# Kernel optimization log

Hardware: AMD Instinct MI355X
Metric: run time of the kernel (lower is better)

Reference implementation:

```python
import jax, jax.numpy as jnp
import numpy as np

D, H = 64, 16
B, S = 4, 4096
PI = 3.1415  # constant used verbatim in the original code


def setup_inputs() -> dict:
    key = jax.random.key(0)
    ks = jax.random.split(key, 11)
    inp = {
        'query': jax.random.normal(ks[0], (B, S, D), dtype=jnp.float32),
        'key': jax.random.normal(ks[1], (B, S, D), dtype=jnp.float32),
        'value': jax.random.normal(ks[2], (B, S, D), dtype=jnp.float32),
        'attn_mask': jnp.zeros((1,), dtype=bool),
        # Linear weights stored as (in, out); y = x @ W + b
        'wq_w': jax.random.normal(ks[3], (D, D * H), dtype=jnp.float32) * 0.05,
        'wq_b': jnp.zeros((D * H,), dtype=jnp.float32),
        'wk_w': jax.random.normal(ks[4], (D, D * H), dtype=jnp.float32) * 0.05,
        'wk_b': jnp.zeros((D * H,), dtype=jnp.float32),
        'wv_w': jax.random.normal(ks[5], (D, D * H), dtype=jnp.float32) * 0.05,
        'wv_b': jnp.zeros((D * H,), dtype=jnp.float32),
        'dense_w': jax.random.normal(ks[6], (D * H, D), dtype=jnp.float32) * 0.05,
        'dense_b': jnp.zeros((D,), dtype=jnp.float32),
    }
    return inp


def reference(query, key, value, attn_mask, wq_w, wq_b, wk_w, wk_b, wv_w, wv_b, dense_w, dense_b):
    b, s, _ = query.shape
    # projections -> (B, S, H, D); einsum axis n = heads
    q = (query @ wq_w + wq_b).reshape(b, s, H, D)
    k = (key @ wk_w + wk_b).reshape(b, s, H, D)
    v = (value @ wv_w + wv_b).reshape(b, s, H, D)

    q = jax.nn.elu(q) + 1.0
    k = jax.nn.elu(k) + 1.0

    pos = PI * jnp.arange(s, dtype=query.dtype) / s  # (S,)
    qc_w = jnp.cos(pos)
    qs_w = jnp.sin(pos)
    kc_w = jnp.sin(pos)  # NB: original uses sin for k_cos too (faithful)
    ks_w = jnp.sin(pos)

    q_cos = q * qc_w[None, :, None, None]
    q_sin = q * qs_w[None, :, None, None]
    k_cos = k * kc_w[None, :, None, None]
    k_sin = k * ks_w[None, :, None, None]

    def lin_attn(qf, kf):
        kv = jnp.einsum('bsnx,bsnz->bnxz', kf, v)      # (B,H,D,D)
        return jnp.einsum('bsnx,bnxz->bsnz', qf, kv)   # (B,S,H,D)

    qkv = lin_attn(q, k)
    qkv_cos = lin_attn(q_cos, k_cos)
    qkv_sin = lin_attn(q_sin, k_sin)

    denom = 1.0 / (
        jnp.einsum('bsnd,bnd->bsn', q, k.sum(axis=1))
        + jnp.einsum('bsnd,bnd->bsn', q_cos, k_cos.sum(axis=1))
        + jnp.einsum('bsnd,bnd->bsn', q_sin, k_sin.sum(axis=1))
        + 1e-05
    )

    O = (qkv + qkv_cos + qkv_sin) * denom[..., None]   # (B,S,H,D)
    concat = O.reshape(b, s, H * D)
    return concat @ dense_w + dense_b
```

## Files before the change

### kernel.cpp

```cpp
#include <hip/hip_runtime.h>
#include <math.h>

#define BB 4
#define SS 4096
#define DD 64
#define HH 16
#define PI_C 3.1415f


typedef __attribute__((ext_vector_type(8))) short short8;
typedef __attribute__((ext_vector_type(4))) float f32x4;

#define MFMA(a, b, c) __builtin_amdgcn_mfma_f32_16x16x32_bf16(a, b, c, 0, 0, 0)

__device__ __forceinline__ short f2bf(float f) {
    union { float f; unsigned u; } v; v.f = f;
    unsigned r = v.u + 0x7FFFu + ((v.u >> 16) & 1u);
    return (short)(r >> 16);
}
__device__ __forceinline__ float bf2f(short s) {
    union { unsigned u; float f; } v;
    v.u = ((unsigned)(unsigned short)s) << 16;
    return v.f;
}
__device__ __forceinline__ short8 cvt8(float4 a, float4 b) {
    short8 r;
    r[0] = f2bf(a.x); r[1] = f2bf(a.y); r[2] = f2bf(a.z); r[3] = f2bf(a.w);
    r[4] = f2bf(b.x); r[5] = f2bf(b.y); r[6] = f2bf(b.z); r[7] = f2bf(b.w);
    return r;
}
__device__ __forceinline__ float elu1(float x) { return x > 0.f ? x + 1.f : __expf(x); }
__device__ __forceinline__ void st4(short* p, short a, short b, short c, short d) {
    union { uint2 u; short s[4]; } x;
    x.s[0] = a; x.s[1] = b; x.s[2] = c; x.s[3] = d;
    *reinterpret_cast<uint2*>(p) = x.u;
}

__global__ __launch_bounds__(256) void k_prep(
    const float* __restrict__ wq, const float* __restrict__ wk,
    const float* __restrict__ wv, const float* __restrict__ wd,
    short* __restrict__ dst)
{
    const int h = blockIdx.x, y = blockIdx.y, t = threadIdx.x;
    const float* src = (y == 0) ? wq : (y == 1) ? wk : (y == 2) ? wv : wd;
    const int rs = (y < 3) ? 1024 : 64;
    const size_t srcbase = (y < 3) ? (size_t)(h * 64) : (size_t)(h * 4096);
    short* dm = dst + (size_t)y * 65536 + (size_t)h * 4096;
#pragma unroll
    for (int j = 0; j < 4; ++j) {
        int idx = j * 1024 + t * 4;
        int r = idx >> 6, c = idx & 63;
        float4 v = *reinterpret_cast<const float4*>(src + (size_t)r * rs + srcbase + c);
        dm[(c + 0) * 64 + r] = f2bf(v.x);
        dm[(c + 1) * 64 + r] = f2bf(v.y);
        dm[(c + 2) * 64 + r] = f2bf(v.z);
        dm[(c + 3) * 64 + r] = f2bf(v.w);
    }
}

__global__ __launch_bounds__(256, 2) void k_phase1(
    const float* __restrict__ key, const float* __restrict__ value,
    const float* __restrict__ wk_b, const float* __restrict__ wv_b,
    const short* __restrict__ wkTb, const short* __restrict__ wvTb,
    float* __restrict__ pkv, float* __restrict__ pkvs,
    float* __restrict__ pks)
{
    const int chunk = blockIdx.x, h = blockIdx.y, b = blockIdx.z;
    const int t = threadIdx.x, w = t >> 6, l = t & 63;
    const int lane15 = l & 15, q8 = (l >> 4) * 8, q4 = (l >> 4) * 4;

    __shared__ short kT[2][64 * 72], vT[2][64 * 72], vsT[2][64 * 72];
    __shared__ float ssin[512];
    __shared__ float sbk[64], sbv[64];
    __shared__ float sred[512];

    short8 bkf[2][4], bvf[2][4];
    {
        const short* wkh = wkTb + (size_t)h * 4096;
        const short* wvh = wvTb + (size_t)h * 4096;
#pragma unroll
        for (int kss = 0; kss < 2; ++kss)
#pragma unroll
            for (int nt = 0; nt < 4; ++nt) {
                bkf[kss][nt] = *reinterpret_cast<const short8*>(wkh + (nt * 16 + lane15) * 64 + kss * 32 + q8);
                bvf[kss][nt] = *reinterpret_cast<const short8*>(wvh + (nt * 16 + lane15) * 64 + kss * 32 + q8);
            }
    }
    ssin[t]       = __sinf(PI_C * (float)(chunk * 512 + t)       * (1.f / 4096.f));
    ssin[t + 256] = __sinf(PI_C * (float)(chunk * 512 + t + 256) * (1.f / 4096.f));
    if (t < 64) sbk[t] = wk_b[h * 64 + t];
    else if (t < 128) sbv[t - 64] = wv_b[h * 64 + (t - 64)];

    float4 kf0, kf1, kf2, kf3, vf0, vf1, vf2, vf3;
    {
        const size_t g = ((size_t)b * SS + chunk * 512 + w * 16 + lane15) * 64 + q8;
        kf0 = *reinterpret_cast<const float4*>(key + g);
        kf1 = *reinterpret_cast<const float4*>(key + g + 4);
        kf2 = *reinterpret_cast<const float4*>(key + g + 32);
        kf3 = *reinterpret_cast<const float4*>(key + g + 36);
        vf0 = *reinterpret_cast<const float4*>(value + g);
        vf1 = *reinterpret_cast<const float4*>(value + g + 4);
        vf2 = *reinterpret_cast<const float4*>(value + g + 32);
        vf3 = *reinterpret_cast<const float4*>(value + g + 36);
    }

    f32x4 ckv[4], ckvs[4];
#pragma unroll
    for (int i = 0; i < 4; ++i) {
        ckv[i]  = (f32x4){0.f, 0.f, 0.f, 0.f};
        ckvs[i] = (f32x4){0.f, 0.f, 0.f, 0.f};
    }
    float aks = 0.f, akss = 0.f;

    auto proj_store = [&](int buf, int sbase) {
        f32x4 ckp[4], cvp[4];
#pragma unroll
        for (int i = 0; i < 4; ++i) {
            ckp[i] = (f32x4){0.f, 0.f, 0.f, 0.f};
            cvp[i] = (f32x4){0.f, 0.f, 0.f, 0.f};
        }
        short8 ak0 = cvt8(kf0, kf1), ak1 = cvt8(kf2, kf3);
        short8 av0 = cvt8(vf0, vf1), av1 = cvt8(vf2, vf3);
#pragma unroll
        for (int nt = 0; nt < 4; ++nt) {
            ckp[nt] = MFMA(ak0, bkf[0][nt], ckp[nt]);
            cvp[nt] = MFMA(av0, bvf[0][nt], cvp[nt]);
            ckp[nt] = MFMA(ak1, bkf[1][nt], ckp[nt]);
            cvp[nt] = MFMA(av1, bvf[1][nt], cvp[nt]);
        }
        const int srel = w * 16 + q4;
#pragma unroll
        for (int nt = 0; nt < 4; ++nt) {
            const int x = nt * 16 + lane15;
            const float bk = sbk[x], bv = sbv[x];
            short ek[4], ev[4], es[4];
#pragma unroll
            for (int r = 0; r < 4; ++r) {
                float kk = elu1(ckp[nt][r] + bk);
                float vv = cvp[nt][r] + bv;
                ek[r] = f2bf(kk);
                ev[r] = f2bf(vv);
                es[r] = f2bf(vv * ssin[sbase + srel + r]);
            }
            st4(&kT [buf][x * 72 + srel], ek[0], ek[1], ek[2], ek[3]);
            st4(&vT [buf][x * 72 + srel], ev[0], ev[1], ev[2], ev[3]);
            st4(&vsT[buf][x * 72 + srel], es[0], es[1], es[2], es[3]);
        }
    };

    __syncthreads();
    proj_store(0, 0);
    __syncthreads();

#pragma unroll 1
    for (int it = 0; it < 8; ++it) {
        const int cur = it & 1;
        if (it < 7) {
            const size_t g = ((size_t)b * SS + chunk * 512 + (it + 1) * 64 + w * 16 + lane15) * 64 + q8;
            kf0 = *reinterpret_cast<const float4*>(key + g);
            kf1 = *reinterpret_cast<const float4*>(key + g + 4);
            kf2 = *reinterpret_cast<const float4*>(key + g + 32);
            kf3 = *reinterpret_cast<const float4*>(key + g + 36);
            vf0 = *reinterpret_cast<const float4*>(value + g);
            vf1 = *reinterpret_cast<const float4*>(value + g + 4);
            vf2 = *reinterpret_cast<const float4*>(value + g + 32);
            vf3 = *reinterpret_cast<const float4*>(value + g + 36);
        }
#pragma unroll
        for (int kstep = 0; kstep < 2; ++kstep) {
            const int so = kstep * 32;
            short8 aV  = *reinterpret_cast<const short8*>(&vT [cur][(w * 16 + lane15) * 72 + so + q8]);
            short8 aVS = *reinterpret_cast<const short8*>(&vsT[cur][(w * 16 + lane15) * 72 + so + q8]);
#pragma unroll
            for (int nt = 0; nt < 4; ++nt) {
                short8 bK = *reinterpret_cast<const short8*>(&kT[cur][(nt * 16 + lane15) * 72 + so + q8]);
                ckv[nt]  = MFMA(aV,  bK, ckv[nt]);
                ckvs[nt] = MFMA(aVS, bK, ckvs[nt]);
            }
        }
        {
            const int sbase = it * 64;
            short8 k0 = *reinterpret_cast<const short8*>(&kT[cur][l * 72 + w * 16]);
            short8 k1 = *reinterpret_cast<const short8*>(&kT[cur][l * 72 + w * 16 + 8]);
#pragma unroll
            for (int e = 0; e < 8; ++e) {
                float fa = bf2f(k0[e]), fb = bf2f(k1[e]);
                aks  += fa + fb;
                akss += fa * ssin[sbase + w * 16 + e] + fb * ssin[sbase + w * 16 + 8 + e];
            }
        }
        if (it < 7) proj_store(cur ^ 1, (it + 1) * 64);
        __syncthreads();
    }

    const int bh = b * HH + h;
    const size_t pbase = ((size_t)(chunk * 64) + bh) * 4096;
#pragma unroll
    for (int nt = 0; nt < 4; ++nt) {
        const int x = nt * 16 + lane15;
#pragma unroll
        for (int r = 0; r < 4; ++r) {
            const int z = w * 16 + q4 + r;
            pkv [pbase + z * 64 + x] = ckv[nt][r];
            pkvs[pbase + z * 64 + x] = ckvs[nt][r];
        }
    }
    sred[t] = aks; sred[256 + t] = akss;
    __syncthreads();
    if (t < 64) {
        pks[((size_t)(chunk * 64) + bh) * 128 + t] =
            sred[t] + sred[64 + t] + sred[128 + t] + sred[192 + t];
    } else if (t < 128) {
        int tt = t - 64;
        pks[((size_t)(chunk * 64) + bh) * 128 + t] =
            sred[256 + tt] + sred[320 + tt] + sred[384 + tt] + sred[448 + tt];
    }
}

__global__ __launch_bounds__(256) void k_reduce(
    const float* __restrict__ pkv, const float* __restrict__ pkvs,
    const float* __restrict__ pks,
    short* __restrict__ kvb, short* __restrict__ kvsb,
    float* __restrict__ ksums)
{
    const int blk = blockIdx.x, t = threadIdx.x;
    if (blk < 512) {
        const float* src = (blk < 256) ? pkv : pkvs;
        short* dst = (blk < 256) ? kvb : kvsb;
        const int o4 = (blk & 255) * 256 + t;
        float4 s = make_float4(0.f, 0.f, 0.f, 0.f);
#pragma unroll
        for (int c = 0; c < 8; ++c) {
            float4 v = reinterpret_cast<const float4*>(src + (size_t)c * 262144)[o4];
            s.x += v.x; s.y += v.y; s.z += v.z; s.w += v.w;
        }
        st4(dst + (size_t)o4 * 4, f2bf(s.x), f2bf(s.y), f2bf(s.z), f2bf(s.w));
    } else {
        const int g = (blk - 512) * 256 + t;
        float4 s = make_float4(0.f, 0.f, 0.f, 0.f);
#pragma unroll
        for (int c = 0; c < 8; ++c) {
            float4 v = reinterpret_cast<const float4*>(pks + (size_t)c * 8192)[g];
            s.x += v.x; s.y += v.y; s.z += v.z; s.w += v.w;
        }
        reinterpret_cast<float4*>(ksums)[g] = s;
    }
}

__global__ __launch_bounds__(256, 2) void k_phase2(
    const float* __restrict__ query, const float* __restrict__ wq_b,
    const short* __restrict__ wqTb,
    const short* __restrict__ kvb, const short* __restrict__ kvsb,
    const float* __restrict__ ksums,
    const short* __restrict__ wdTb, const float* __restrict__ dense_b,
    float* __restrict__ out)
{
    const int st = blockIdx.x, b = blockIdx.y;
    const int s0 = st * 32;
    const int t = threadIdx.x, w = t >> 6, l = t & 63;
    const int lane15 = l & 15, q8 = (l >> 4) * 8, q4 = (l >> 4) * 4;

    __shared__ __align__(16) char smem[34816];
    __shared__ float scc[32];
    short* sqin = reinterpret_cast<short*>(smem);
    short* sqp  = reinterpret_cast<short*>(smem) + 2304 * (1 + w);
    short* sOw  = reinterpret_cast<short*>(smem) + 2304 * 5 + 1152 * w;

    {
        const int row = t >> 3, c8 = (t & 7) * 8;
        const float* qp = query + ((size_t)b * SS + s0 + row) * 64 + c8;
        float4 f0 = *reinterpret_cast<const float4*>(qp);
        float4 f1 = *reinterpret_cast<const float4*>(qp + 4);
        *reinterpret_cast<short8*>(&sqin[row * 72 + c8]) = cvt8(f0, f1);
    }
    if (t < 32) {
        float p = PI_C * (float)(s0 + t) * (1.f / 4096.f);
        scc[t] = __cosf(p) + __sinf(p);
    }
    f32x4 cd[2][4];
#pragma unroll
    for (int rt = 0; rt < 2; ++rt)
#pragma unroll
        for (int nt = 0; nt < 4; ++nt) cd[rt][nt] = (f32x4){0.f, 0.f, 0.f, 0.f};
    __syncthreads();

    short8 aq[2][2];
#pragma unroll
    for (int rt = 0; rt < 2; ++rt)
#pragma unroll
        for (int kss = 0; kss < 2; ++kss)
            aq[rt][kss] = *reinterpret_cast<const short8*>(&sqin[(rt * 16 + lane15) * 72 + kss * 32 + q8]);
    const float ccs0 = scc[lane15], ccs1 = scc[16 + lane15];
    const int drow = l >> 1, dxh = (l & 1) * 32;
    const float ccr = scc[drow];

#pragma unroll 1
    for (int i = 0; i < 4; ++i) {
        const int h = (i << 2) | w;
        const size_t bh = (size_t)(b * HH + h);
        const short* wqh = wqTb + (size_t)h * 4096;
        const short* wdh = wdTb + (size_t)h * 4096;
        const short* kv1 = kvb  + bh * 4096;
        const short* kv2 = kvsb + bh * 4096;

        f32x4 cq[2][4];
#pragma unroll
        for (int rt = 0; rt < 2; ++rt)
#pragma unroll
            for (int nt = 0; nt < 4; ++nt) cq[rt][nt] = (f32x4){0.f, 0.f, 0.f, 0.f};
#pragma unroll
        for (int nt = 0; nt < 4; ++nt) {
            short8 b0 = *reinterpret_cast<const short8*>(wqh + (nt * 16 + lane15) * 64 + q8);
            short8 b1 = *reinterpret_cast<const short8*>(wqh + (nt * 16 + lane15) * 64 + 32 + q8);
            cq[0][nt] = MFMA(b0, aq[0][0], cq[0][nt]);
            cq[1][nt] = MFMA(b0, aq[1][0], cq[1][nt]);
            cq[0][nt] = MFMA(b1, aq[0][1], cq[0][nt]);
            cq[1][nt] = MFMA(b1, aq[1][1], cq[1][nt]);
        }
#pragma unroll
        for (int nt = 0; nt < 4; ++nt) {
            float4 bq = *reinterpret_cast<const float4*>(wq_b + h * 64 + nt * 16 + q4);
#pragma unroll
            for (int rt = 0; rt < 2; ++rt) {
                short e0 = f2bf(elu1(cq[rt][nt][0] + bq.x));
                short e1 = f2bf(elu1(cq[rt][nt][1] + bq.y));
                short e2 = f2bf(elu1(cq[rt][nt][2] + bq.z));
                short e3 = f2bf(elu1(cq[rt][nt][3] + bq.w));
                st4(&sqp[(rt * 16 + lane15) * 72 + nt * 16 + q4], e0, e1, e2, e3);
            }
        }

        float invs0, invs1;
        {
            const float* kp = ksums + bh * 128 + dxh;
            float4 A[8], Bv[8];
#pragma unroll
            for (int j = 0; j < 8; ++j) {
                A[j]  = *reinterpret_cast<const float4*>(kp + j * 4);
                Bv[j] = *reinterpret_cast<const float4*>(kp + 64 + j * 4);
            }
            short8 qr[4];
#pragma unroll
            for (int e = 0; e < 4; ++e)
                qr[e] = *reinterpret_cast<const short8*>(&sqp[drow * 72 + dxh + e * 8]);
            float dsum = 0.f;
#pragma unroll
            for (int j4 = 0; j4 < 8; ++j4)
#pragma unroll
                for (int e4 = 0; e4 < 4; ++e4)
                    dsum += bf2f(qr[j4 >> 1][(j4 & 1) * 4 + e4]) * (A[j4][e4] + ccr * Bv[j4][e4]);
            dsum += __shfl_xor(dsum, 1);
            float invd = 1.f / (dsum + 1e-5f);
            invs0 = __shfl(invd, lane15 * 2);
            invs1 = __shfl(invd, (16 + lane15) * 2);
        }

        short8 qf[2][2];
#pragma unroll
        for (int rt = 0; rt < 2; ++rt)
#pragma unroll
            for (int kss = 0; kss < 2; ++kss)
                qf[rt][kss] = *reinterpret_cast<const short8*>(&sqp[(rt * 16 + lane15) * 72 + kss * 32 + q8]);
        f32x4 cv1[2][4], cv2[2][4];
#pragma unroll
        for (int rt = 0; rt < 2; ++rt)
#pragma unroll
            for (int nt = 0; nt < 4; ++nt) {
                cv1[rt][nt] = (f32x4){0.f, 0.f, 0.f, 0.f};
                cv2[rt][nt] = (f32x4){0.f, 0.f, 0.f, 0.f};
            }
#pragma unroll
        for (int nt = 0; nt < 4; ++nt) {
            const short* a1 = kv1 + (nt * 16 + lane15) * 64;
            const short* a2 = kv2 + (nt * 16 + lane15) * 64;
            short8 f10 = *reinterpret_cast<const short8*>(a1 + q8);
            short8 f11 = *reinterpret_cast<const short8*>(a1 + 32 + q8);
            short8 f20 = *reinterpret_cast<const short8*>(a2 + q8);
            short8 f21 = *reinterpret_cast<const short8*>(a2 + 32 + q8);
#pragma unroll
            for (int rt = 0; rt < 2; ++rt) {
                cv1[rt][nt] = MFMA(f10, qf[rt][0], cv1[rt][nt]);
                cv1[rt][nt] = MFMA(f11, qf[rt][1], cv1[rt][nt]);
                cv2[rt][nt] = MFMA(f20, qf[rt][0], cv2[rt][nt]);
                cv2[rt][nt] = MFMA(f21, qf[rt][1], cv2[rt][nt]);
            }
        }
        short8 wdf[4][2];
#pragma unroll
        for (int nt = 0; nt < 4; ++nt)
#pragma unroll
            for (int kss = 0; kss < 2; ++kss)
                wdf[nt][kss] = *reinterpret_cast<const short8*>(wdh + (nt * 16 + lane15) * 64 + kss * 32 + q8);

#pragma unroll
        for (int rt = 0; rt < 2; ++rt) {
            const float ccsr = rt ? ccs1 : ccs0;
            const float invr = rt ? invs1 : invs0;
#pragma unroll
            for (int nt = 0; nt < 4; ++nt) {
                short e0 = f2bf((cv1[rt][nt][0] + ccsr * cv2[rt][nt][0]) * invr);
                short e1 = f2bf((cv1[rt][nt][1] + ccsr * cv2[rt][nt][1]) * invr);
                short e2 = f2bf((cv1[rt][nt][2] + ccsr * cv2[rt][nt][2]) * invr);
                short e3 = f2bf((cv1[rt][nt][3] + ccsr * cv2[rt][nt][3]) * invr);
                st4(&sOw[lane15 * 72 + nt * 16 + q4], e0, e1, e2, e3);
            }
            short8 of0 = *reinterpret_cast<const short8*>(&sOw[lane15 * 72 + q8]);
            short8 of1 = *reinterpret_cast<const short8*>(&sOw[lane15 * 72 + 32 + q8]);
#pragma unroll
            for (int nt = 0; nt < 4; ++nt) {
                cd[rt][nt] = MFMA(of0, wdf[nt][0], cd[rt][nt]);
                cd[rt][nt] = MFMA(of1, wdf[nt][1], cd[rt][nt]);
            }
        }
    }

    __syncthreads();
    {
        float* red = reinterpret_cast<float*>(smem) + 2176 * w;
#pragma unroll
        for (int rt = 0; rt < 2; ++rt)
#pragma unroll
            for (int nt = 0; nt < 4; ++nt)
#pragma unroll
                for (int r = 0; r < 4; ++r)
                    red[(rt * 16 + q4 + r) * 68 + nt * 16 + lane15] = cd[rt][nt][r];
    }
    __syncthreads();
    {
        const int row = t >> 3, c8 = (t & 7) * 8;
        float4 sa = make_float4(0.f, 0.f, 0.f, 0.f);
        float4 sb = make_float4(0.f, 0.f, 0.f, 0.f);
#pragma unroll
        for (int ww = 0; ww < 4; ++ww) {
            const float* red = reinterpret_cast<const float*>(smem) + 2176 * ww;
            float4 v0 = *reinterpret_cast<const float4*>(red + row * 68 + c8);
            float4 v1 = *reinterpret_cast<const float4*>(red + row * 68 + c8 + 4);
            sa.x += v0.x; sa.y += v0.y; sa.z += v0.z; sa.w += v0.w;
            sb.x += v1.x; sb.y += v1.y; sb.z += v1.z; sb.w += v1.w;
        }
        float4 d0 = *reinterpret_cast<const float4*>(dense_b + c8);
        float4 d1 = *reinterpret_cast<const float4*>(dense_b + c8 + 4);
        sa.x += d0.x; sa.y += d0.y; sa.z += d0.z; sa.w += d0.w;
        sb.x += d1.x; sb.y += d1.y; sb.z += d1.z; sb.w += d1.w;
        float* op = out + ((size_t)b * SS + s0 + row) * 64 + c8;
        *reinterpret_cast<float4*>(op)     = sa;
        *reinterpret_cast<float4*>(op + 4) = sb;
    }
}

extern "C" void kernel_launch(void* const* d_in, const int* in_sizes, int n_in,
                              void* d_out, int out_size, void* d_ws, size_t ws_size,
                              hipStream_t stream) {
    const float* query   = (const float*)d_in[0];
    const float* key     = (const float*)d_in[1];
    const float* value   = (const float*)d_in[2];
    const float* wq_w    = (const float*)d_in[4];
    const float* wq_b    = (const float*)d_in[5];
    const float* wk_w    = (const float*)d_in[6];
    const float* wk_b    = (const float*)d_in[7];
    const float* wv_w    = (const float*)d_in[8];
    const float* wv_b    = (const float*)d_in[9];
    const float* dense_w = (const float*)d_in[10];
    const float* dense_b = (const float*)d_in[11];
    float* out = (float*)d_out;

    char* ws = (char*)d_ws;
    float* pkv   = (float*)(ws);
    float* pkvs  = (float*)(ws + 8388608);
    float* pks   = (float*)(ws + 16777216);
    short* kvb   = (short*)(ws + 17039360);
    short* kvsb  = (short*)(ws + 17563648);
    float* ksums = (float*)(ws + 18087936);
    short* wT    = (short*)(ws + 18120704);
    short* wqTb  = wT;
    short* wkTb  = wT + 65536;
    short* wvTb  = wT + 131072;
    short* wdTb  = wT + 196608;

    hipLaunchKernelGGL(k_prep, dim3(16, 4), dim3(256), 0, stream,
                       wq_w, wk_w, wv_w, dense_w, wT);
    hipLaunchKernelGGL(k_phase1, dim3(8, HH, BB), dim3(256), 0, stream,
                       key, value, wk_b, wv_b, wkTb, wvTb, pkv, pkvs, pks);
    hipLaunchKernelGGL(k_reduce, dim3(520), dim3(256), 0, stream,
                       pkv, pkvs, pks, kvb, kvsb, ksums);
    hipLaunchKernelGGL(k_phase2, dim3(128, BB), dim3(256), 0, stream,
                       query, wq_b, wqTb, kvb, kvsb, ksums, wdTb, dense_b, out);
}
```

Baseline: 152.6 us.

## Double block size to 512 threads and specialize waves for K vs V projection

```diff
diff --git a/kernel.cpp b/kernel.cpp
--- a/kernel.cpp
+++ b/kernel.cpp
@@ -58,7 +58,7 @@
     }
 }
 
-__global__ __launch_bounds__(256, 2) void k_phase1(
+__global__ __launch_bounds__(512, 4) void k_phase1(
     const float* __restrict__ key, const float* __restrict__ value,
     const float* __restrict__ wk_b, const float* __restrict__ wv_b,
     const short* __restrict__ wkTb, const short* __restrict__ wvTb,
@@ -68,120 +68,121 @@
     const int chunk = blockIdx.x, h = blockIdx.y, b = blockIdx.z;
     const int t = threadIdx.x, w = t >> 6, l = t & 63;
     const int lane15 = l & 15, q8 = (l >> 4) * 8, q4 = (l >> 4) * 4;
-
-    __shared__ short kT[2][64 * 72], vT[2][64 * 72], vsT[2][64 * 72];
+    const int wk4 = w & 3;
+    const bool isK = (w < 4);
+
+    __shared__ short kT[64 * 136], vT[64 * 136], vsT[64 * 136];
     __shared__ float ssin[512];
     __shared__ float sbk[64], sbv[64];
-    __shared__ float sred[512];
-
-    short8 bkf[2][4], bvf[2][4];
+    __shared__ float sred[1024];
+
+    const float* src = isK ? key : value;
+    const size_t gbase = ((size_t)b * SS + chunk * 512) * 64;
+
+    float4 pf[2][4];
+#pragma unroll
+    for (int s2 = 0; s2 < 2; ++s2) {
+        const size_t g = gbase + (size_t)(wk4 * 32 + s2 * 16 + lane15) * 64 + q8;
+        pf[s2][0] = *reinterpret_cast<const float4*>(src + g);
+        pf[s2][1] = *reinterpret_cast<const float4*>(src + g + 4);
+        pf[s2][2] = *reinterpret_cast<const float4*>(src + g + 32);
+        pf[s2][3] = *reinterpret_cast<const float4*>(src + g + 36);
+    }
+
+    short8 bwf[2][4];
     {
-        const short* wkh = wkTb + (size_t)h * 4096;
-        const short* wvh = wvTb + (size_t)h * 4096;
+        const short* wh = (isK ? wkTb : wvTb) + (size_t)h * 4096;
 #pragma unroll
         for (int kss = 0; kss < 2; ++kss)
 #pragma unroll
-            for (int nt = 0; nt < 4; ++nt) {
-                bkf[kss][nt] = *reinterpret_cast<const short8*>(wkh + (nt * 16 + lane15) * 64 + kss * 32 + q8);
-                bvf[kss][nt] = *reinterpret_cast<const short8*>(wvh + (nt * 16 + lane15) * 64 + kss * 32 + q8);
-            }
-    }
-    ssin[t]       = __sinf(PI_C * (float)(chunk * 512 + t)       * (1.f / 4096.f));
-    ssin[t + 256] = __sinf(PI_C * (float)(chunk * 512 + t + 256) * (1.f / 4096.f));
+            for (int nt = 0; nt < 4; ++nt)
+                bwf[kss][nt] = *reinterpret_cast<const short8*>(wh + (nt * 16 + lane15) * 64 + kss * 32 + q8);
+    }
+    ssin[t] = __sinf(PI_C * (float)(chunk * 512 + t) * (1.f / 4096.f));
     if (t < 64) sbk[t] = wk_b[h * 64 + t];
     else if (t < 128) sbv[t - 64] = wv_b[h * 64 + (t - 64)];
 
-    float4 kf0, kf1, kf2, kf3, vf0, vf1, vf2, vf3;
-    {
-        const size_t g = ((size_t)b * SS + chunk * 512 + w * 16 + lane15) * 64 + q8;
-        kf0 = *reinterpret_cast<const float4*>(key + g);
-        kf1 = *reinterpret_cast<const float4*>(key + g + 4);
-        kf2 = *reinterpret_cast<const float4*>(key + g + 32);
-        kf3 = *reinterpret_cast<const float4*>(key + g + 36);
-        vf0 = *reinterpret_cast<const float4*>(value + g);
-        vf1 = *reinterpret_cast<const float4*>(value + g + 4);
-        vf2 = *reinterpret_cast<const float4*>(value + g + 32);
-        vf3 = *reinterpret_cast<const float4*>(value + g + 36);
-    }
-
-    f32x4 ckv[4], ckvs[4];
-#pragma unroll
-    for (int i = 0; i < 4; ++i) {
-        ckv[i]  = (f32x4){0.f, 0.f, 0.f, 0.f};
-        ckvs[i] = (f32x4){0.f, 0.f, 0.f, 0.f};
-    }
+    f32x4 cacc[4];
+#pragma unroll
+    for (int i = 0; i < 4; ++i) cacc[i] = (f32x4){0.f, 0.f, 0.f, 0.f};
     float aks = 0.f, akss = 0.f;
 
-    auto proj_store = [&](int buf, int sbase) {
-        f32x4 ckp[4], cvp[4];
-#pragma unroll
-        for (int i = 0; i < 4; ++i) {
-            ckp[i] = (f32x4){0.f, 0.f, 0.f, 0.f};
-            cvp[i] = (f32x4){0.f, 0.f, 0.f, 0.f};
-        }
-        short8 ak0 = cvt8(kf0, kf1), ak1 = cvt8(kf2, kf3);
-        short8 av0 = cvt8(vf0, vf1), av1 = cvt8(vf2, vf3);
-#pragma unroll
-        for (int nt = 0; nt < 4; ++nt) {
-            ckp[nt] = MFMA(ak0, bkf[0][nt], ckp[nt]);
-            cvp[nt] = MFMA(av0, bvf[0][nt], cvp[nt]);
-            ckp[nt] = MFMA(ak1, bkf[1][nt], ckp[nt]);
-            cvp[nt] = MFMA(av1, bvf[1][nt], cvp[nt]);
-        }
-        const int srel = w * 16 + q4;
-#pragma unroll
-        for (int nt = 0; nt < 4; ++nt) {
-            const int x = nt * 16 + lane15;
-            const float bk = sbk[x], bv = sbv[x];
-            short ek[4], ev[4], es[4];
-#pragma unroll
-            for (int r = 0; r < 4; ++r) {
-                float kk = elu1(ckp[nt][r] + bk);
-                float vv = cvp[nt][r] + bv;
-                ek[r] = f2bf(kk);
-                ev[r] = f2bf(vv);
-                es[r] = f2bf(vv * ssin[sbase + srel + r]);
-            }
-            st4(&kT [buf][x * 72 + srel], ek[0], ek[1], ek[2], ek[3]);
-            st4(&vT [buf][x * 72 + srel], ev[0], ev[1], ev[2], ev[3]);
-            st4(&vsT[buf][x * 72 + srel], es[0], es[1], es[2], es[3]);
-        }
-    };
-
+    short8 a0[2], a1[2];
+#pragma unroll
+    for (int s2 = 0; s2 < 2; ++s2) {
+        a0[s2] = cvt8(pf[s2][0], pf[s2][1]);
+        a1[s2] = cvt8(pf[s2][2], pf[s2][3]);
+    }
     __syncthreads();
-    proj_store(0, 0);
-    __syncthreads();
 
 #pragma unroll 1
-    for (int it = 0; it < 8; ++it) {
-        const int cur = it & 1;
-        if (it < 7) {
-            const size_t g = ((size_t)b * SS + chunk * 512 + (it + 1) * 64 + w * 16 + lane15) * 64 + q8;
-            kf0 = *reinterpret_cast<const float4*>(key + g);
-            kf1 = *reinterpret_cast<const float4*>(key + g + 4);
-            kf2 = *reinterpret_cast<const float4*>(key + g + 32);
-            kf3 = *reinterpret_cast<const float4*>(key + g + 36);
-            vf0 = *reinterpret_cast<const float4*>(value + g);
-            vf1 = *reinterpret_cast<const float4*>(value + g + 4);
-            vf2 = *reinterpret_cast<const float4*>(value + g + 32);
-            vf3 = *reinterpret_cast<const float4*>(value + g + 36);
-        }
-#pragma unroll
-        for (int kstep = 0; kstep < 2; ++kstep) {
-            const int so = kstep * 32;
-            short8 aV  = *reinterpret_cast<const short8*>(&vT [cur][(w * 16 + lane15) * 72 + so + q8]);
-            short8 aVS = *reinterpret_cast<const short8*>(&vsT[cur][(w * 16 + lane15) * 72 + so + q8]);
+    for (int it = 0; it < 4; ++it) {
+        const int sbase = it * 128;
+#pragma unroll
+        for (int s2 = 0; s2 < 2; ++s2) {
+            f32x4 cp[4];
+#pragma unroll
+            for (int i = 0; i < 4; ++i) cp[i] = (f32x4){0.f, 0.f, 0.f, 0.f};
 #pragma unroll
             for (int nt = 0; nt < 4; ++nt) {
-                short8 bK = *reinterpret_cast<const short8*>(&kT[cur][(nt * 16 + lane15) * 72 + so + q8]);
-                ckv[nt]  = MFMA(aV,  bK, ckv[nt]);
-                ckvs[nt] = MFMA(aVS, bK, ckvs[nt]);
+                cp[nt] = MFMA(a0[s2], bwf[0][nt], cp[nt]);
+                cp[nt] = MFMA(a1[s2], bwf[1][nt], cp[nt]);
+            }
+            const int srel = wk4 * 32 + s2 * 16 + q4;
+            if (isK) {
+#pragma unroll
+                for (int nt = 0; nt < 4; ++nt) {
+                    const int x = nt * 16 + lane15;
+                    const float bk = sbk[x];
+                    short ek[4];
+#pragma unroll
+                    for (int r = 0; r < 4; ++r) ek[r] = f2bf(elu1(cp[nt][r] + bk));
+                    st4(&kT[x * 136 + srel], ek[0], ek[1], ek[2], ek[3]);
+                }
+            } else {
+#pragma unroll
+                for (int nt = 0; nt < 4; ++nt) {
+                    const int x = nt * 16 + lane15;
+                    const float bv = sbv[x];
+                    short ev[4], es[4];
+#pragma unroll
+                    for (int r = 0; r < 4; ++r) {
+                        float vv = cp[nt][r] + bv;
+                        ev[r] = f2bf(vv);
+                        es[r] = f2bf(vv * ssin[sbase + srel + r]);
+                    }
+                    st4(&vT [x * 136 + srel], ev[0], ev[1], ev[2], ev[3]);
+                    st4(&vsT[x * 136 + srel], es[0], es[1], es[2], es[3]);
+                }
+            }
+        }
+        __syncthreads();
+        if (it < 3) {
+#pragma unroll
+            for (int s2 = 0; s2 < 2; ++s2) {
+                const size_t g = gbase + (size_t)((it + 1) * 128 + wk4 * 32 + s2 * 16 + lane15) * 64 + q8;
+                pf[s2][0] = *reinterpret_cast<const float4*>(src + g);
+                pf[s2][1] = *reinterpret_cast<const float4*>(src + g + 4);
+                pf[s2][2] = *reinterpret_cast<const float4*>(src + g + 32);
+                pf[s2][3] = *reinterpret_cast<const float4*>(src + g + 36);
             }
         }
         {
-            const int sbase = it * 64;
-            short8 k0 = *reinterpret_cast<const short8*>(&kT[cur][l * 72 + w * 16]);
-            short8 k1 = *reinterpret_cast<const short8*>(&kT[cur][l * 72 + w * 16 + 8]);
+            const short* aSrc = isK ? vT : vsT;
+#pragma unroll
+            for (int ks = 0; ks < 4; ++ks) {
+                const int so = ks * 32;
+                short8 aV = *reinterpret_cast<const short8*>(&aSrc[(wk4 * 16 + lane15) * 136 + so + q8]);
+#pragma unroll
+                for (int nt = 0; nt < 4; ++nt) {
+                    short8 bK = *reinterpret_cast<const short8*>(&kT[(nt * 16 + lane15) * 136 + so + q8]);
+                    cacc[nt] = MFMA(aV, bK, cacc[nt]);
+                }
+            }
+        }
+        {
+            short8 k0 = *reinterpret_cast<const short8*>(&kT[l * 136 + w * 16]);
+            short8 k1 = *reinterpret_cast<const short8*>(&kT[l * 136 + w * 16 + 8]);
 #pragma unroll
             for (int e = 0; e < 8; ++e) {
                 float fa = bf2f(k0[e]), fb = bf2f(k1[e]);
@@ -189,31 +190,41 @@
                 akss += fa * ssin[sbase + w * 16 + e] + fb * ssin[sbase + w * 16 + 8 + e];
             }
         }
-        if (it < 7) proj_store(cur ^ 1, (it + 1) * 64);
+        if (it < 3) {
+#pragma unroll
+            for (int s2 = 0; s2 < 2; ++s2) {
+                a0[s2] = cvt8(pf[s2][0], pf[s2][1]);
+                a1[s2] = cvt8(pf[s2][2], pf[s2][3]);
+            }
+        }
         __syncthreads();
     }
 
     const int bh = b * HH + h;
     const size_t pbase = ((size_t)(chunk * 64) + bh) * 4096;
+    float* dst = isK ? pkv : pkvs;
 #pragma unroll
     for (int nt = 0; nt < 4; ++nt) {
         const int x = nt * 16 + lane15;
 #pragma unroll
         for (int r = 0; r < 4; ++r) {
-            const int z = w * 16 + q4 + r;
-            pkv [pbase + z * 64 + x] = ckv[nt][r];
-            pkvs[pbase + z * 64 + x] = ckvs[nt][r];
-        }
-    }
-    sred[t] = aks; sred[256 + t] = akss;
+            const int z = wk4 * 16 + q4 + r;
+            dst[pbase + z * 64 + x] = cacc[nt][r];
+        }
+    }
+    sred[t] = aks; sred[512 + t] = akss;
     __syncthreads();
     if (t < 64) {
-        pks[((size_t)(chunk * 64) + bh) * 128 + t] =
-            sred[t] + sred[64 + t] + sred[128 + t] + sred[192 + t];
+        float s = 0.f;
+#pragma unroll
+        for (int j = 0; j < 8; ++j) s += sred[j * 64 + t];
+        pks[((size_t)(chunk * 64) + bh) * 128 + t] = s;
     } else if (t < 128) {
-        int tt = t - 64;
-        pks[((size_t)(chunk * 64) + bh) * 128 + t] =
-            sred[256 + tt] + sred[320 + tt] + sred[384 + tt] + sred[448 + tt];
+        const int tt = t - 64;
+        float s = 0.f;
+#pragma unroll
+        for (int j = 0; j < 8; ++j) s += sred[512 + j * 64 + tt];
+        pks[((size_t)(chunk * 64) + bh) * 128 + 64 + tt] = s;
     }
 }
 
@@ -247,7 +258,7 @@
     }
 }
 
-__global__ __launch_bounds__(256, 2) void k_phase2(
+__global__ __launch_bounds__(512, 4) void k_phase2(
     const float* __restrict__ query, const float* __restrict__ wq_b,
     const short* __restrict__ wqTb,
     const short* __restrict__ kvb, const short* __restrict__ kvsb,
@@ -260,18 +271,15 @@
     const int t = threadIdx.x, w = t >> 6, l = t & 63;
     const int lane15 = l & 15, q8 = (l >> 4) * 8, q4 = (l >> 4) * 4;
 
-    __shared__ __align__(16) char smem[34816];
+    __shared__ __align__(16) char smem[41472];
     __shared__ float scc[32];
     short* sqin = reinterpret_cast<short*>(smem);
     short* sqp  = reinterpret_cast<short*>(smem) + 2304 * (1 + w);
-    short* sOw  = reinterpret_cast<short*>(smem) + 2304 * 5 + 1152 * w;
 
     {
-        const int row = t >> 3, c8 = (t & 7) * 8;
-        const float* qp = query + ((size_t)b * SS + s0 + row) * 64 + c8;
-        float4 f0 = *reinterpret_cast<const float4*>(qp);
-        float4 f1 = *reinterpret_cast<const float4*>(qp + 4);
-        *reinterpret_cast<short8*>(&sqin[row * 72 + c8]) = cvt8(f0, f1);
+        const int row = t >> 4, c4 = (t & 15) * 4;
+        float4 f = *reinterpret_cast<const float4*>(query + ((size_t)b * SS + s0 + row) * 64 + c4);
+        st4(&sqin[row * 72 + c4], f2bf(f.x), f2bf(f.y), f2bf(f.z), f2bf(f.w));
     }
     if (t < 32) {
         float p = PI_C * (float)(s0 + t) * (1.f / 4096.f);
@@ -295,8 +303,8 @@
     const float ccr = scc[drow];
 
 #pragma unroll 1
-    for (int i = 0; i < 4; ++i) {
-        const int h = (i << 2) | w;
+    for (int i = 0; i < 2; ++i) {
+        const int h = i * 8 + w;
         const size_t bh = (size_t)(b * HH + h);
         const short* wqh = wqTb + (size_t)h * 4096;
         const short* wdh = wdTb + (size_t)h * 4096;
@@ -402,10 +410,10 @@
                 short e1 = f2bf((cv1[rt][nt][1] + ccsr * cv2[rt][nt][1]) * invr);
                 short e2 = f2bf((cv1[rt][nt][2] + ccsr * cv2[rt][nt][2]) * invr);
                 short e3 = f2bf((cv1[rt][nt][3] + ccsr * cv2[rt][nt][3]) * invr);
-                st4(&sOw[lane15 * 72 + nt * 16 + q4], e0, e1, e2, e3);
-            }
-            short8 of0 = *reinterpret_cast<const short8*>(&sOw[lane15 * 72 + q8]);
-            short8 of1 = *reinterpret_cast<const short8*>(&sOw[lane15 * 72 + 32 + q8]);
+                st4(&sqp[(rt * 16 + lane15) * 72 + nt * 16 + q4], e0, e1, e2, e3);
+            }
+            short8 of0 = *reinterpret_cast<const short8*>(&sqp[(rt * 16 + lane15) * 72 + q8]);
+            short8 of1 = *reinterpret_cast<const short8*>(&sqp[(rt * 16 + lane15) * 72 + 32 + q8]);
 #pragma unroll
             for (int nt = 0; nt < 4; ++nt) {
                 cd[rt][nt] = MFMA(of0, wdf[nt][0], cd[rt][nt]);
@@ -416,35 +424,43 @@
 
     __syncthreads();
     {
-        float* red = reinterpret_cast<float*>(smem) + 2176 * w;
-#pragma unroll
-        for (int rt = 0; rt < 2; ++rt)
-#pragma unroll
-            for (int nt = 0; nt < 4; ++nt)
-#pragma unroll
-                for (int r = 0; r < 4; ++r)
-                    red[(rt * 16 + q4 + r) * 68 + nt * 16 + lane15] = cd[rt][nt][r];
+        float* red = reinterpret_cast<float*>(smem) + 2176 * (w & 3);
+        if (w < 4) {
+#pragma unroll
+            for (int rt = 0; rt < 2; ++rt)
+#pragma unroll
+                for (int nt = 0; nt < 4; ++nt)
+#pragma unroll
+                    for (int r = 0; r < 4; ++r)
+                        red[(rt * 16 + q4 + r) * 68 + nt * 16 + lane15] = cd[rt][nt][r];
+        }
     }
     __syncthreads();
     {
-        const int row = t >> 3, c8 = (t & 7) * 8;
-        float4 sa = make_float4(0.f, 0.f, 0.f, 0.f);
-        float4 sb = make_float4(0.f, 0.f, 0.f, 0.f);
+        float* red = reinterpret_cast<float*>(smem) + 2176 * (w & 3);
+        if (w >= 4) {
+#pragma unroll
+            for (int rt = 0; rt < 2; ++rt)
+#pragma unroll
+                for (int nt = 0; nt < 4; ++nt)
+#pragma unroll
+                    for (int r = 0; r < 4; ++r)
+                        red[(rt * 16 + q4 + r) * 68 + nt * 16 + lane15] += cd[rt][nt][r];
+        }
+    }
+    __syncthreads();
+    {
+        const int row = t >> 4, c4 = (t & 15) * 4;
+        float4 s = make_float4(0.f, 0.f, 0.f, 0.f);
 #pragma unroll
         for (int ww = 0; ww < 4; ++ww) {
             const float* red = reinterpret_cast<const float*>(smem) + 2176 * ww;
-            float4 v0 = *reinterpret_cast<const float4*>(red + row * 68 + c8);
-            float4 v1 = *reinterpret_cast<const float4*>(red + row * 68 + c8 + 4);
-            sa.x += v0.x; sa.y += v0.y; sa.z += v0.z; sa.w += v0.w;
-            sb.x += v1.x; sb.y += v1.y; sb.z += v1.z; sb.w += v1.w;
-        }
-        float4 d0 = *reinterpret_cast<const float4*>(dense_b + c8);
-        float4 d1 = *reinterpret_cast<const float4*>(dense_b + c8 + 4);
-        sa.x += d0.x; sa.y += d0.y; sa.z += d0.z; sa.w += d0.w;
-        sb.x += d1.x; sb.y += d1.y; sb.z += d1.z; sb.w += d1.w;
-        float* op = out + ((size_t)b * SS + s0 + row) * 64 + c8;
-        *reinterpret_cast<float4*>(op)     = sa;
-        *reinterpret_cast<float4*>(op + 4) = sb;
+            float4 v = *reinterpret_cast<const float4*>(red + row * 68 + c4);
+            s.x += v.x; s.y += v.y; s.z += v.z; s.w += v.w;
+        }
+        float4 db = *reinterpret_cast<const float4*>(dense_b + c4);
+        s.x += db.x; s.y += db.y; s.z += db.z; s.w += db.w;
+        *reinterpret_cast<float4*>(out + ((size_t)b * SS + s0 + row) * 64 + c4) = s;
     }
 }
 
@@ -479,10 +495,10 @@
 
     hipLaunchKernelGGL(k_prep, dim3(16, 4), dim3(256), 0, stream,
                        wq_w, wk_w, wv_w, dense_w, wT);
-    hipLaunchKernelGGL(k_phase1, dim3(8, HH, BB), dim3(256), 0, stream,
+    hipLaunchKernelGGL(k_phase1, dim3(8, HH, BB), dim3(512), 0, stream,
                        key, value, wk_b, wv_b, wkTb, wvTb, pkv, pkvs, pks);
     hipLaunchKernelGGL(k_reduce, dim3(520), dim3(256), 0, stream,
                        pkv, pkvs, pks, kvb, kvsb, ksums);
-    hipLaunchKernelGGL(k_phase2, dim3(128, BB), dim3(256), 0, stream,
+    hipLaunchKernelGGL(k_phase2, dim3(128, BB), dim3(512), 0, stream,
                        query, wq_b, wqTb, kvb, kvsb, ksums, wdTb, dense_b, out);
 }
```

Measured after the change: 216.5 us. 41.9% more time.

## Split phase2 heads across two block groups and combine partial outputs

Applied to the files above, without the earlier changes.

```diff
diff --git a/kernel.cpp b/kernel.cpp
--- a/kernel.cpp
+++ b/kernel.cpp
@@ -252,10 +252,10 @@
     const short* __restrict__ wqTb,
     const short* __restrict__ kvb, const short* __restrict__ kvsb,
     const float* __restrict__ ksums,
-    const short* __restrict__ wdTb, const float* __restrict__ dense_b,
-    float* __restrict__ out)
+    const short* __restrict__ wdTb,
+    float* __restrict__ pout)
 {
-    const int st = blockIdx.x, b = blockIdx.y;
+    const int st = blockIdx.x, g = blockIdx.y, b = blockIdx.z;
     const int s0 = st * 32;
     const int t = threadIdx.x, w = t >> 6, l = t & 63;
     const int lane15 = l & 15, q8 = (l >> 4) * 8, q4 = (l >> 4) * 4;
@@ -295,8 +295,8 @@
     const float ccr = scc[drow];
 
 #pragma unroll 1
-    for (int i = 0; i < 4; ++i) {
-        const int h = (i << 2) | w;
+    for (int i = 0; i < 2; ++i) {
+        const int h = (g << 3) | (i << 2) | w;
         const size_t bh = (size_t)(b * HH + h);
         const short* wqh = wqTb + (size_t)h * 4096;
         const short* wdh = wdTb + (size_t)h * 4096;
@@ -438,14 +438,27 @@
             sa.x += v0.x; sa.y += v0.y; sa.z += v0.z; sa.w += v0.w;
             sb.x += v1.x; sb.y += v1.y; sb.z += v1.z; sb.w += v1.w;
         }
-        float4 d0 = *reinterpret_cast<const float4*>(dense_b + c8);
-        float4 d1 = *reinterpret_cast<const float4*>(dense_b + c8 + 4);
-        sa.x += d0.x; sa.y += d0.y; sa.z += d0.z; sa.w += d0.w;
-        sb.x += d1.x; sb.y += d1.y; sb.z += d1.z; sb.w += d1.w;
-        float* op = out + ((size_t)b * SS + s0 + row) * 64 + c8;
+        float* op = pout + (size_t)g * (BB * SS * 64)
+                  + ((size_t)b * SS + s0 + row) * 64 + c8;
         *reinterpret_cast<float4*>(op)     = sa;
         *reinterpret_cast<float4*>(op + 4) = sb;
     }
+}
+
+__global__ __launch_bounds__(256) void k_combine(
+    const float* __restrict__ pout, const float* __restrict__ dense_b,
+    float* __restrict__ out)
+{
+    const int o = blockIdx.x * 256 + threadIdx.x;
+    float4 a = reinterpret_cast<const float4*>(pout)[o];
+    float4 c = reinterpret_cast<const float4*>(pout + (size_t)BB * SS * 64)[o];
+    float4 db = reinterpret_cast<const float4*>(dense_b)[o & 15];
+    float4 r;
+    r.x = a.x + c.x + db.x;
+    r.y = a.y + c.y + db.y;
+    r.z = a.z + c.z + db.z;
+    r.w = a.w + c.w + db.w;
+    reinterpret_cast<float4*>(out)[o] = r;
 }
 
 extern "C" void kernel_launch(void* const* d_in, const int* in_sizes, int n_in,
@@ -476,6 +489,7 @@
     short* wkTb  = wT + 65536;
     short* wvTb  = wT + 131072;
     short* wdTb  = wT + 196608;
+    float* pout  = pkv;
 
     hipLaunchKernelGGL(k_prep, dim3(16, 4), dim3(256), 0, stream,
                        wq_w, wk_w, wv_w, dense_w, wT);
@@ -483,6 +497,8 @@
                        key, value, wk_b, wv_b, wkTb, wvTb, pkv, pkvs, pks);
     hipLaunchKernelGGL(k_reduce, dim3(520), dim3(256), 0, stream,
                        pkv, pkvs, pks, kvb, kvsb, ksums);
-    hipLaunchKernelGGL(k_phase2, dim3(128, BB), dim3(256), 0, stream,
-                       query, wq_b, wqTb, kvb, kvsb, ksums, wdTb, dense_b, out);
-}
+    hipLaunchKernelGGL(k_phase2, dim3(128, 2, BB), dim3(256), 0, stream,
+                       query, wq_b, wqTb, kvb, kvsb, ksums, wdTb, pout);
+    hipLaunchKernelGGL(k_combine, dim3(1024), dim3(256), 0, stream,
+                       pout, dense_b, out);
+}
```

Measured after the change: 159.9 us. 4.8% more time.
